# Kernel optimization log

Hardware: AMD Instinct MI355X
Metric: run time of the kernel (lower is better)

Reference implementation:

```python
import jax, jax.numpy as jnp
import numpy as np

B, C, H, W = 8, 64, 112, 112
KEY_NUM = 9


def conv1x1(x, w, b):
    # x: [b,c,h,w], w: [co,ci], b: [co]
    return jnp.einsum('bchw,oc->bohw', x, w) + b[None, :, None, None]


def bilinear_sample(feat, dy, dx):
    # feat: [b,c,H,W]; dy,dx: [b,H,W]. Zero-padded bilinear point sampling
    # (equivalent to torchvision deform_conv2d with 1x1 identity weight).
    b, c, h, w = feat.shape
    yy = jnp.arange(h, dtype=feat.dtype)[:, None]
    xx = jnp.arange(w, dtype=feat.dtype)[None, :]
    py = dy + yy  # [b,h,w]
    px = dx + xx
    y0 = jnp.floor(py)
    x0 = jnp.floor(px)
    wy1 = py - y0
    wx1 = px - x0
    wy0 = 1.0 - wy1
    wx0 = 1.0 - wx1
    featf = feat.reshape(b, c, h * w)

    def gather(yi, xi):
        valid = (yi >= 0) & (yi < h) & (xi >= 0) & (xi < w)
        yc = jnp.clip(yi, 0, h - 1).astype(jnp.int32)
        xc = jnp.clip(xi, 0, w - 1).astype(jnp.int32)
        idx = (yc * w + xc).reshape(b, 1, h * w)
        v = jnp.take_along_axis(featf, idx, axis=2).reshape(b, c, h, w)
        return v * valid.astype(feat.dtype)[:, None]

    return (gather(y0, x0) * (wy0 * wx0)[:, None]
            + gather(y0, x0 + 1) * (wy0 * wx1)[:, None]
            + gather(y0 + 1, x0) * (wy1 * wx0)[:, None]
            + gather(y0 + 1, x0 + 1) * (wy1 * wx1)[:, None])


def setup_inputs() -> dict:
    key = jax.random.key(0)
    ks = jax.random.split(key, 8)
    s = 1.0 / np.sqrt(C)
    return {
        'query_layer': jax.random.normal(ks[0], (B, C, H, W), jnp.float32),
        'key_layer': jax.random.normal(ks[1], (B, C, H, W), jnp.float32),
        'w_refer': jax.random.normal(ks[2], (C, C), jnp.float32) * s,
        'b_refer': jax.random.normal(ks[3], (C,), jnp.float32) * 0.1,
        'w_attn': jax.random.normal(ks[4], (KEY_NUM, C), jnp.float32) * s,
        'b_attn': jax.random.normal(ks[5], (KEY_NUM,), jnp.float32) * 0.1,
        'w_off': jax.random.normal(ks[6], (2 * KEY_NUM, C), jnp.float32) * s,
        'b_off': jax.random.normal(ks[7], (2 * KEY_NUM,), jnp.float32) * 0.1,
    }


def reference(query_layer, key_layer, w_refer, b_refer, w_attn, b_attn, w_off, b_off):
    key_feature = conv1x1(key_layer, w_refer, b_refer)          # [b,c,h,w]
    attn = jax.nn.softmax(conv1x1(query_layer, w_attn, b_attn), axis=1)  # [b,K,h,w]
    offset = conv1x1(query_layer, w_off, b_off)                  # [b,2K,h,w]
    # Faithful to original: key k uses offset channels [k, k+1] (overlapping slices)
    dys = jnp.moveaxis(offset[:, 0:KEY_NUM], 1, 0)               # [K,b,h,w]
    dxs = jnp.moveaxis(offset[:, 1:KEY_NUM + 1], 1, 0)           # [K,b,h,w]
    sampled = jax.vmap(bilinear_sample, in_axes=(None, 0, 0))(key_feature, dys, dxs)  # [K,b,c,h,w]
    out = jnp.einsum('kbchw,bkhw->bchw', sampled, attn)
    return out
```

## Files before the change

### kernel.cpp

```cpp
#include <hip/hip_runtime.h>
#include <hip/hip_fp16.h>

#define BB 8
#define CC 64
#define HH 112
#define WW 112
#define HWs (HH * WW)
#define KEYN 9

#define CK_PX 128
#define CK_TILES (HWs / CK_PX)
#define CK_NBLK (BB * CK_TILES)
#define WTS 68

#define SM_PX 32
#define SM_TILES (HWs / SM_PX)
#define SM_NBLK (BB * SM_TILES)

#define OFF_WQ   0
#define OFF_SB   1280
#define OFF_L    1300
#define OFF_XQ   1972
#define OFF_P    0
#define OFF_T    0
#define OFF_OUTT 2304
#define SM_LDS   4480

__device__ __forceinline__ float swzx16(float v) {
    return __uint_as_float(__builtin_amdgcn_ds_swizzle(__float_as_uint(v), 0x401F));
}
__device__ __forceinline__ float swzx8(float v) {
    return __uint_as_float(__builtin_amdgcn_ds_swizzle(__float_as_uint(v), 0x201F));
}

__global__ __launch_bounds__(256, 4) void conv_key_kernel(
    const float* __restrict__ key, const float* __restrict__ w_refer,
    const float* __restrict__ b_refer, __half* __restrict__ Kf)
{
    __shared__ float Wt[64 * WTS];

    const int t = threadIdx.x;
    const int blk = blockIdx.x;
    const int b = blk & 7;
    const int s0 = (blk >> 3) * CK_PX;
    const size_t inb = (size_t)b * CC * HWs + s0;

    #pragma unroll
    for (int m = 0; m < 4; ++m) {
        const int f = t + 256 * m;
        const int o = f >> 4;
        const int q = f & 15;
        const float4 wv = *reinterpret_cast<const float4*>(w_refer + o * CC + 4 * q);
        Wt[(4 * q + 0) * WTS + o] = wv.x;
        Wt[(4 * q + 1) * WTS + o] = wv.y;
        Wt[(4 * q + 2) * WTS + o] = wv.z;
        Wt[(4 * q + 3) * WTS + o] = wv.w;
    }
    __syncthreads();

    const int og = t & 7;
    const int p4 = t >> 3;
    const float4 bias0 = *reinterpret_cast<const float4*>(b_refer + 8 * og);
    const float4 bias1 = *reinterpret_cast<const float4*>(b_refer + 8 * og + 4);
    float4 acc[4][2];
    #pragma unroll
    for (int pi = 0; pi < 4; ++pi) { acc[pi][0] = bias0; acc[pi][1] = bias1; }

    #pragma unroll 4
    for (int k = 0; k < 64; ++k) {
        const float4 a4 = *reinterpret_cast<const float4*>(key + inb + (size_t)k * HWs + 4 * p4);
        const float4 w0 = *reinterpret_cast<const float4*>(&Wt[k * WTS + 8 * og]);
        const float4 w1 = *reinterpret_cast<const float4*>(&Wt[k * WTS + 8 * og + 4]);
        const float ap[4] = {a4.x, a4.y, a4.z, a4.w};
        #pragma unroll
        for (int pi = 0; pi < 4; ++pi) {
            acc[pi][0].x = fmaf(ap[pi], w0.x, acc[pi][0].x);
            acc[pi][0].y = fmaf(ap[pi], w0.y, acc[pi][0].y);
            acc[pi][0].z = fmaf(ap[pi], w0.z, acc[pi][0].z);
            acc[pi][0].w = fmaf(ap[pi], w0.w, acc[pi][0].w);
            acc[pi][1].x = fmaf(ap[pi], w1.x, acc[pi][1].x);
            acc[pi][1].y = fmaf(ap[pi], w1.y, acc[pi][1].y);
            acc[pi][1].z = fmaf(ap[pi], w1.z, acc[pi][1].z);
            acc[pi][1].w = fmaf(ap[pi], w1.w, acc[pi][1].w);
        }
    }

    #pragma unroll
    for (int pi = 0; pi < 4; ++pi) {
        const size_t ob = ((size_t)b * HWs + s0 + 4 * p4 + pi) * CC + 8 * og;
        union { __half2 h; int i; } u0, u1, u2, u3;
        u0.h = __floats2half2_rn(acc[pi][0].x, acc[pi][0].y);
        u1.h = __floats2half2_rn(acc[pi][0].z, acc[pi][0].w);
        u2.h = __floats2half2_rn(acc[pi][1].x, acc[pi][1].y);
        u3.h = __floats2half2_rn(acc[pi][1].z, acc[pi][1].w);
        int4 pk; pk.x = u0.i; pk.y = u1.i; pk.z = u2.i; pk.w = u3.i;
        *reinterpret_cast<int4*>(Kf + ob) = pk;
    }
}

struct TEnt { float4 a, b; };

__device__ __forceinline__ TEnt make_entry2(int e, float4 pk, int s0)
{
    const int p = e & 31;
    const int s = s0 + p;
    const int yi = s / WW;
    const int xi = s - yi * WW;
    const float py  = pk.y + (float)yi;
    const float pxf = pk.z + (float)xi;
    const float fy = floorf(py), fx = floorf(pxf);
    const float wy1 = py - fy, wx1 = pxf - fx;
    const float wy0 = 1.f - wy1, wx0 = 1.f - wx1;
    const int ix0 = (int)fx;
    const int iy0 = (int)fy, iy1 = iy0 + 1;
    const float vx0 = (ix0 >= 0 && ix0 < WW)      ? 1.f : 0.f;
    const float vx1 = (ix0 >= -1 && ix0 < WW - 1) ? 1.f : 0.f;
    const float vy0 = (iy0 >= 0 && iy0 < HH)      ? 1.f : 0.f;
    const float vy1 = (iy1 >= 0 && iy1 < HH)      ? 1.f : 0.f;
    const int yc0 = min(max(iy0, 0), HH - 1);
    const int yc1 = min(max(iy1, 0), HH - 1);
    TEnt r;
    r.a.x = __uint_as_float((unsigned)(yc0 * WW * 128));
    r.a.y = __uint_as_float((unsigned)(yc1 * WW * 128));
    r.a.z = __int_as_float(ix0);
    r.a.w = 0.f;
    const float ay0 = pk.x * wy0 * vy0;
    const float ay1 = pk.x * wy1 * vy1;
    r.b.x = ay0 * wx0 * vx0;
    r.b.y = ay0 * wx1 * vx1;
    r.b.z = ay1 * wx0 * vx0;
    r.b.w = ay1 * wx1 * vx1;
    return r;
}

__global__ __launch_bounds__(256, 8) void fused_sample_kernel(
    const float* __restrict__ query, const float* __restrict__ w_attn,
    const float* __restrict__ b_attn, const float* __restrict__ w_off,
    const float* __restrict__ b_off, const __half* __restrict__ Kf,
    float* __restrict__ out)
{
    __shared__ float S[SM_LDS];
    float*  Wq   = S + OFF_WQ;
    float*  Sb   = S + OFF_SB;
    float*  L    = S + OFF_L;
    float*  Xq   = S + OFF_XQ;
    float4* Pf4  = reinterpret_cast<float4*>(S + OFF_P);
    float*  Tb   = S + OFF_T;
    float*  OutT = S + OFF_OUTT;

    const int t = threadIdx.x;
    const int l = t & 63;
    const int w = t >> 6;
    const int blk = blockIdx.x;
    const int b = blk & 7;
    const int tile = blk >> 3;
    const int s0 = tile * SM_PX;
    const size_t qb = (size_t)b * CC * HWs + s0;
    const char* Kfb = reinterpret_cast<const char*>(Kf) + (size_t)b * HWs * 128;

    for (int f = t; f < 304; f += 256) {
        const int r = f >> 4;
        const int q = f & 15;
        const float* src = (r < KEYN) ? (w_attn + r * CC) : (w_off + (r - KEYN) * CC);
        const float4 wv = *reinterpret_cast<const float4*>(src + 4 * q);
        Wq[(4 * q + 0) * 20 + r] = wv.x;
        Wq[(4 * q + 1) * 20 + r] = wv.y;
        Wq[(4 * q + 2) * 20 + r] = wv.z;
        Wq[(4 * q + 3) * 20 + r] = wv.w;
    }
    if (t < 64) Wq[t * 20 + 19] = 0.f;
    if (t < 20) Sb[t] = (t < KEYN) ? b_attn[t] : (t < 19 ? b_off[t - KEYN] : 0.f);
    #pragma unroll
    for (int m = 0; m < 2; ++m) {
        const int f = t + 256 * m;
        const int c = f >> 3;
        const int p4 = (f & 7) * 4;
        *reinterpret_cast<float4*>(&Xq[c * 32 + p4]) =
            *reinterpret_cast<const float4*>(query + qb + (size_t)c * HWs + p4);
    }
    __syncthreads();

    {
        const int px = t & 31;
        const int og = t >> 5;
        if (og < 5) {
            const int o4 = 4 * og;
            float4 acc = *reinterpret_cast<const float4*>(&Sb[o4]);
            #pragma unroll 8
            for (int k = 0; k < 64; ++k) {
                const float a = Xq[k * 32 + px];
                const float4 wv = *reinterpret_cast<const float4*>(&Wq[k * 20 + o4]);
                acc.x = fmaf(a, wv.x, acc.x);
                acc.y = fmaf(a, wv.y, acc.y);
                acc.z = fmaf(a, wv.z, acc.z);
                acc.w = fmaf(a, wv.w, acc.w);
            }
            L[px * 21 + o4 + 0] = acc.x;
            L[px * 21 + o4 + 1] = acc.y;
            L[px * 21 + o4 + 2] = acc.z;
            L[px * 21 + o4 + 3] = acc.w;
        }
    }
    __syncthreads();

    if (t < SM_PX) {
        float lg[KEYN], of[10];
        #pragma unroll
        for (int k = 0; k < KEYN; ++k) lg[k] = L[t * 21 + k];
        #pragma unroll
        for (int j = 0; j < 10; ++j) of[j] = L[t * 21 + KEYN + j];
        float m = lg[0];
        #pragma unroll
        for (int k = 1; k < KEYN; ++k) m = fmaxf(m, lg[k]);
        float s = 0.f, e[KEYN];
        #pragma unroll
        for (int k = 0; k < KEYN; ++k) { e[k] = expf(lg[k] - m); s += e[k]; }
        const float sinv = 1.0f / s;
        #pragma unroll
        for (int k = 0; k < KEYN; ++k)
            Pf4[k * 32 + t] = make_float4(e[k] * sinv, of[k], of[k + 1], 0.f);
    }
    __syncthreads();

    {
        const float4 q1 = Pf4[t];
        float4 q2 = make_float4(0.f, 0.f, 0.f, 0.f);
        if (t < 32) q2 = Pf4[256 + t];
        __syncthreads();
        const TEnt e1 = make_entry2(t, q1, s0);
        *reinterpret_cast<float4*>(Tb + t * 8)     = e1.a;
        *reinterpret_cast<float4*>(Tb + t * 8 + 4) = e1.b;
        if (t < 32) {
            const TEnt e2 = make_entry2(256 + t, q2, s0);
            *reinterpret_cast<float4*>(Tb + (256 + t) * 8)     = e2.a;
            *reinterpret_cast<float4*>(Tb + (256 + t) * 8 + 4) = e2.b;
        }
    }
    __syncthreads();

    const int  ch8  = l & 7;
    const bool c2b  = (l >> 3) & 1;
    const bool rowb = (l >> 4) & 1;
    const int  sub  = l >> 5;
    const unsigned chb = (unsigned)(ch8 * 16);

    for (int j = 0; j < 4; ++j) {
        const int p = w * 8 + 2 * j + sub;
        const float* Te = Tb + p * 8;

        float acc[8] = {0.f, 0.f, 0.f, 0.f, 0.f, 0.f, 0.f, 0.f};
        #pragma unroll
        for (int k = 0; k < KEYN; ++k) {
            const float4 t1 = *reinterpret_cast<const float4*>(Te + k * 256);
            const float4 t2 = *reinterpret_cast<const float4*>(Te + k * 256 + 4);
            const int xi = __float_as_int(t1.z) + (c2b ? 1 : 0);
            const int xc = min(max(xi, 0), WW - 1);
            const unsigned rb = __float_as_uint(rowb ? t1.y : t1.x);
            const float wgt = rowb ? (c2b ? t2.w : t2.z) : (c2b ? t2.y : t2.x);
            const unsigned addr = rb + ((unsigned)xc << 7) + chb;
            const int4 raw = *reinterpret_cast<const int4*>(Kfb + addr);
            union { int i; __half2 h; } u0, u1, u2, u3;
            u0.i = raw.x; u1.i = raw.y; u2.i = raw.z; u3.i = raw.w;
            acc[0] = fmaf(__low2float(u0.h),  wgt, acc[0]);
            acc[1] = fmaf(__high2float(u0.h), wgt, acc[1]);
            acc[2] = fmaf(__low2float(u1.h),  wgt, acc[2]);
            acc[3] = fmaf(__high2float(u1.h), wgt, acc[3]);
            acc[4] = fmaf(__low2float(u2.h),  wgt, acc[4]);
            acc[5] = fmaf(__high2float(u2.h), wgt, acc[5]);
            acc[6] = fmaf(__low2float(u3.h),  wgt, acc[6]);
            acc[7] = fmaf(__high2float(u3.h), wgt, acc[7]);
        }

        #pragma unroll
        for (int i = 0; i < 8; ++i) acc[i] += swzx16(acc[i]);
        #pragma unroll
        for (int i = 0; i < 8; ++i) acc[i] += swzx8(acc[i]);

        if ((l & 24) == 0) {
            float* d = OutT + p * 68 + ch8 * 8;
            *reinterpret_cast<float4*>(d)     = make_float4(acc[0], acc[1], acc[2], acc[3]);
            *reinterpret_cast<float4*>(d + 4) = make_float4(acc[4], acc[5], acc[6], acc[7]);
        }
    }
    __syncthreads();

    const size_t ob = (size_t)b * CC * HWs + s0;
    #pragma unroll
    for (int m = 0; m < 8; ++m) {
        const int f = t + 256 * m;
        const int c = f >> 5;
        const int px = f & 31;
        out[ob + (size_t)c * HWs + px] = OutT[px * 68 + c];
    }
}

extern "C" void kernel_launch(void* const* d_in, const int* in_sizes, int n_in,
                              void* d_out, int out_size, void* d_ws, size_t ws_size,
                              hipStream_t stream)
{
    const float* query   = (const float*)d_in[0];
    const float* key     = (const float*)d_in[1];
    const float* w_refer = (const float*)d_in[2];
    const float* b_refer = (const float*)d_in[3];
    const float* w_attn  = (const float*)d_in[4];
    const float* b_attn  = (const float*)d_in[5];
    const float* w_off   = (const float*)d_in[6];
    const float* b_off   = (const float*)d_in[7];
    float* out = (float*)d_out;

    __half* Kf = (__half*)d_ws;

    hipLaunchKernelGGL(conv_key_kernel, dim3(CK_NBLK), dim3(256), 0, stream,
                       key, w_refer, b_refer, Kf);
    hipLaunchKernelGGL(fused_sample_kernel, dim3(SM_NBLK), dim3(256), 0, stream,
                       query, w_attn, b_attn, w_off, b_off, Kf, out);
}
```

Before: 148.3 us.

## Stage key tile in LDS, precompute corner addresses, batch gather loads via inline asm

The key conv kernel now copies its input tile into shared memory before the FMA loop instead of reading global memory on every k iteration. In the sample kernel, the table entries are rewritten per pixel with precomputed clamped per-corner addresses and weights, laid out so each lane reads one float2 per key. All nine gathers are then issued as inline-asm global_load_dwordx4 before a single wait, which increases memory-level parallelism. Launch bounds are lowered on both kernels to leave room for the extra registers and LDS, at the cost of occupancy.

Result: no change. 147.1 us (-0.8%).

```diff
diff --git a/kernel.cpp b/kernel.cpp
--- a/kernel.cpp
+++ b/kernel.cpp
@@ -26,6 +26,11 @@
 #define OFF_OUTT 2304
 #define SM_LDS   4480
 
+typedef int v4i __attribute__((ext_vector_type(4)));
+
+#define GLOAD(dst, p) asm volatile("global_load_dwordx4 %0, %1, off" \
+                                   : "=&v"(dst) : "v"(p))
+
 __device__ __forceinline__ float swzx16(float v) {
     return __uint_as_float(__builtin_amdgcn_ds_swizzle(__float_as_uint(v), 0x401F));
 }
@@ -33,10 +38,11 @@
     return __uint_as_float(__builtin_amdgcn_ds_swizzle(__float_as_uint(v), 0x201F));
 }
 
-__global__ __launch_bounds__(256, 4) void conv_key_kernel(
+__global__ __launch_bounds__(256, 3) void conv_key_kernel(
     const float* __restrict__ key, const float* __restrict__ w_refer,
     const float* __restrict__ b_refer, __half* __restrict__ Kf)
 {
+    __shared__ float Xin[64 * CK_PX];
     __shared__ float Wt[64 * WTS];
 
     const int t = threadIdx.x;
@@ -56,6 +62,14 @@
         Wt[(4 * q + 2) * WTS + o] = wv.z;
         Wt[(4 * q + 3) * WTS + o] = wv.w;
     }
+    #pragma unroll
+    for (int m = 0; m < 8; ++m) {
+        const int f = t + 256 * m;
+        const int k = f >> 5;
+        const int p8 = f & 31;
+        *reinterpret_cast<float4*>(&Xin[k * CK_PX + 4 * p8]) =
+            *reinterpret_cast<const float4*>(key + inb + (size_t)k * HWs + 4 * p8);
+    }
     __syncthreads();
 
     const int og = t & 7;
@@ -68,7 +82,7 @@
 
     #pragma unroll 4
     for (int k = 0; k < 64; ++k) {
-        const float4 a4 = *reinterpret_cast<const float4*>(key + inb + (size_t)k * HWs + 4 * p4);
+        const float4 a4 = *reinterpret_cast<const float4*>(&Xin[k * CK_PX + 4 * p4]);
         const float4 w0 = *reinterpret_cast<const float4*>(&Wt[k * WTS + 8 * og]);
         const float4 w1 = *reinterpret_cast<const float4*>(&Wt[k * WTS + 8 * og + 4]);
         const float ap[4] = {a4.x, a4.y, a4.z, a4.w};
@@ -133,7 +147,7 @@
     return r;
 }
 
-__global__ __launch_bounds__(256, 8) void fused_sample_kernel(
+__global__ __launch_bounds__(256, 4) void fused_sample_kernel(
     const float* __restrict__ query, const float* __restrict__ w_attn,
     const float* __restrict__ b_attn, const float* __restrict__ w_off,
     const float* __restrict__ b_off, const __half* __restrict__ Kf,
@@ -227,40 +241,56 @@
         float4 q2 = make_float4(0.f, 0.f, 0.f, 0.f);
         if (t < 32) q2 = Pf4[256 + t];
         __syncthreads();
-        const TEnt e1 = make_entry2(t, q1, s0);
-        *reinterpret_cast<float4*>(Tb + t * 8)     = e1.a;
-        *reinterpret_cast<float4*>(Tb + t * 8 + 4) = e1.b;
-        if (t < 32) {
-            const TEnt e2 = make_entry2(256 + t, q2, s0);
-            *reinterpret_cast<float4*>(Tb + (256 + t) * 8)     = e2.a;
-            *reinterpret_cast<float4*>(Tb + (256 + t) * 8 + 4) = e2.b;
+        #pragma unroll
+        for (int m = 0; m < 2; ++m) {
+            const int e = (m == 0) ? t : (256 + t);
+            if (m == 1 && t >= 32) break;
+            const TEnt en = make_entry2(e, (m == 0) ? q1 : q2, s0);
+            const int p = e & 31, k = e >> 5;
+            const int x0 = __float_as_int(en.a.z);
+            const unsigned xc0 = (unsigned)(min(max(x0, 0), WW - 1)) << 7;
+            const unsigned xc1 = (unsigned)(min(max(x0 + 1, 0), WW - 1)) << 7;
+            const unsigned rb0 = __float_as_uint(en.a.x);
+            const unsigned rb1 = __float_as_uint(en.a.y);
+            float4 r0, r1;
+            r0.x = __uint_as_float(rb0 + xc0); r0.y = en.b.x;
+            r0.z = __uint_as_float(rb0 + xc1); r0.w = en.b.y;
+            r1.x = __uint_as_float(rb1 + xc0); r1.y = en.b.z;
+            r1.z = __uint_as_float(rb1 + xc1); r1.w = en.b.w;
+            float* dst = Tb + (p * 9 + k) * 8;
+            *reinterpret_cast<float4*>(dst)     = r0;
+            *reinterpret_cast<float4*>(dst + 4) = r1;
         }
     }
     __syncthreads();
 
     const int  ch8  = l & 7;
-    const bool c2b  = (l >> 3) & 1;
-    const bool rowb = (l >> 4) & 1;
+    const int  corf = ((l >> 3) & 3) * 2;
     const int  sub  = l >> 5;
-    const unsigned chb = (unsigned)(ch8 * 16);
+    const char* KfbC = Kfb + (unsigned)(ch8 * 16);
 
     for (int j = 0; j < 4; ++j) {
         const int p = w * 8 + 2 * j + sub;
-        const float* Te = Tb + p * 8;
+        const float* Te = Tb + p * 72 + corf;
+
+        float2 tw[KEYN];
+        #pragma unroll
+        for (int k = 0; k < KEYN; ++k)
+            tw[k] = *reinterpret_cast<const float2*>(Te + k * 8);
+
+        v4i rr[KEYN];
+        #pragma unroll
+        for (int k = 0; k < KEYN; ++k)
+            GLOAD(rr[k], KfbC + __float_as_uint(tw[k].x));
+        asm volatile("s_waitcnt vmcnt(0)" ::: "memory");
+        __builtin_amdgcn_sched_barrier(0);
 
         float acc[8] = {0.f, 0.f, 0.f, 0.f, 0.f, 0.f, 0.f, 0.f};
         #pragma unroll
         for (int k = 0; k < KEYN; ++k) {
-            const float4 t1 = *reinterpret_cast<const float4*>(Te + k * 256);
-            const float4 t2 = *reinterpret_cast<const float4*>(Te + k * 256 + 4);
-            const int xi = __float_as_int(t1.z) + (c2b ? 1 : 0);
-            const int xc = min(max(xi, 0), WW - 1);
-            const unsigned rb = __float_as_uint(rowb ? t1.y : t1.x);
-            const float wgt = rowb ? (c2b ? t2.w : t2.z) : (c2b ? t2.y : t2.x);
-            const unsigned addr = rb + ((unsigned)xc << 7) + chb;
-            const int4 raw = *reinterpret_cast<const int4*>(Kfb + addr);
+            const float wgt = tw[k].y;
             union { int i; __half2 h; } u0, u1, u2, u3;
-            u0.i = raw.x; u1.i = raw.y; u2.i = raw.z; u3.i = raw.w;
+            u0.i = rr[k][0]; u1.i = rr[k][1]; u2.i = rr[k][2]; u3.i = rr[k][3];
             acc[0] = fmaf(__low2float(u0.h),  wgt, acc[0]);
             acc[1] = fmaf(__high2float(u0.h), wgt, acc[1]);
             acc[2] = fmaf(__low2float(u1.h),  wgt, acc[2]);
```
